# Performance work log

Hardware: AMD Instinct MI355X
Metric: run time of the kernel (lower is better)

## Reference

```python
import jax, jax.numpy as jnp
import numpy as np

EPS = 1e-8  # torch F.cosine_similarity eps
TEMP = 1.0  # temperature k


def setup_inputs() -> dict:
    key = jax.random.key(0)
    k1, k2, k3 = jax.random.split(key, 3)
    B, T, N, D = 16, 4096, 512, 512
    c = jax.random.normal(k1, (B, T, D), dtype=jnp.float32)
    y_t = jax.random.normal(k2, (B, T, D), dtype=jnp.float32)
    y_distraction = jax.random.normal(k3, (B, N, D), dtype=jnp.float32)
    return {"c": c, "y_t": y_t, "y_distraction": y_distraction}


def reference(c, y_t, y_distraction):
    # norms clamped at eps, matching torch F.cosine_similarity
    n_c = jnp.maximum(jnp.linalg.norm(c, axis=-1), EPS)            # [B,T]
    n_t = jnp.maximum(jnp.linalg.norm(y_t, axis=-1), EPS)          # [B,T]
    n_d = jnpp_norm = jnp.maximum(jnp.linalg.norm(y_distraction, axis=-1), EPS)  # [B,N]

    # positive similarity and exp
    q_t = jnp.exp(jnp.sum(y_t * c, axis=-1) / (n_t * n_c) / TEMP)  # [B,T]

    # distractor cosine similarities via einsum (avoids [B,T,N,D] broadcast)
    scores = jnp.einsum('btd,bnd->btn', c, y_distraction)          # [B,T,N]
    scores = scores / (n_c[:, :, None] * n_d[:, None, :])
    q_distraction = jnp.sum(jnp.exp(scores / TEMP), axis=2) + q_t  # [B,T]

    loss = -jnp.sum(jnp.log(q_t / q_distraction))                  # scalar
    return loss
```

## Files before the change

### kernel.cpp

```cpp
#include <hip/hip_runtime.h>
#include <hip/hip_bf16.h>

#define B_   16
#define T_   4096
#define N_   512
#define D_   512
#define EPSF 1e-8f

typedef __attribute__((ext_vector_type(8))) short bf16x8;
typedef __attribute__((ext_vector_type(4))) float f32x4;

__device__ __forceinline__ unsigned int pack2bf(float a, float b) {
  unsigned int ua = __float_as_uint(a);
  ua += 0x7fffu + ((ua >> 16) & 1u);
  unsigned int ub = __float_as_uint(b);
  ub += 0x7fffu + ((ub >> 16) & 1u);
  return (ua >> 16) | (ub & 0xffff0000u);
}

__device__ __forceinline__ void gload_lds16(const void* g, void* l) {
  __builtin_amdgcn_global_load_lds(
      (const __attribute__((address_space(1))) unsigned int*)g,
      (__attribute__((address_space(3))) unsigned int*)l, 16, 0, 0);
}

__global__ void rownorms_d(const float* __restrict__ yd,
                           float* __restrict__ inv_nd,
                           unsigned short* __restrict__ ydbf) {
  const int tid = threadIdx.x;
  const int g   = tid >> 4;
  const int t   = tid & 15;
  const int row = blockIdx.x * 16 + g;
  const float* dr = yd + (size_t)row * D_;
  unsigned short* ob = ydbf + (size_t)row * D_;

  float dd = 0.f;
#pragma unroll
  for (int k = 0; k < 8; ++k) {
    const int col = k * 64 + t * 4;
    float4 a = *(const float4*)(dr + col);
    dd += a.x * a.x + a.y * a.y + a.z * a.z + a.w * a.w;
    uint2 p;
    p.x = pack2bf(a.x, a.y);
    p.y = pack2bf(a.z, a.w);
    *(uint2*)(ob + col) = p;
  }
#pragma unroll
  for (int m = 1; m < 16; m <<= 1) dd += __shfl_xor(dd, m);
  if (t == 0) inv_nd[row] = 1.f / fmaxf(sqrtf(dd), EPSF);
}

__launch_bounds__(512, 2)
__global__ void fused_ct(const float* __restrict__ c,
                         const float* __restrict__ yt,
                         const unsigned short* __restrict__ ydbf,
                         const float* __restrict__ inv_nd,
                         float* __restrict__ rt,
                         float* __restrict__ S) {
  __shared__ __align__(16) unsigned char As[128 * 64 * 2];
  __shared__ __align__(16) unsigned char Bs[512 * 64 * 2];
  __shared__ float s_invc[128];
  __shared__ float s_invd[512];

  const int mt = blockIdx.x;
  const int b  = blockIdx.y;
  const int tid  = threadIdx.x;
  const int lane = tid & 63;
  const int w    = tid >> 6;
  const int wm   = w >> 2, wn = w & 3;

  const float* Ab = c  + ((size_t)b * T_ + (size_t)mt * 128) * D_;
  const float* Tb = yt + ((size_t)b * T_ + (size_t)mt * 128) * D_;
  const unsigned short* Bb = ydbf + (size_t)b * N_ * D_;

#pragma unroll
  for (int j = 0; j < 8; ++j) {
    const int g   = j * 512 + tid;
    const int row = g >> 3;
    const int sch = (g & 7) ^ (row & 7);
    gload_lds16(Bb + (size_t)row * D_ + (sch << 3), Bs + (g << 4));
  }

  s_invd[tid] = inv_nd[b * N_ + tid];

  {
    const int t  = tid & 15;
    const int rg = tid >> 4;
#pragma unroll
    for (int rp = 0; rp < 4; ++rp) {
      const int row = rp * 32 + rg;
      const float* cr = Ab + (size_t)row * D_;
      const float* tr = Tb + (size_t)row * D_;
      float cc = 0.f, tt = 0.f, ct = 0.f;
#pragma unroll
      for (int k = 0; k < 8; ++k) {
        const int col = k * 64 + t * 4;
        float4 a  = *(const float4*)(cr + col);
        float4 bb = *(const float4*)(tr + col);
        cc += a.x * a.x + a.y * a.y + a.z * a.z + a.w * a.w;
        tt += bb.x * bb.x + bb.y * bb.y + bb.z * bb.z + bb.w * bb.w;
        ct += a.x * bb.x + a.y * bb.y + a.z * bb.z + a.w * bb.w;
      }
#pragma unroll
      for (int m = 1; m < 16; m <<= 1) {
        cc += __shfl_xor(cc, m);
        tt += __shfl_xor(tt, m);
        ct += __shfl_xor(ct, m);
      }
      if (t == 0) {
        float nc = fmaxf(sqrtf(cc), EPSF);
        float nt = fmaxf(sqrtf(tt), EPSF);
        s_invc[row] = 1.f / nc;
        rt[b * T_ + mt * 128 + row] = ct / (nt * nc);
      }
    }
  }

  f32x4 acc[4][8] = {};

  for (int k0i = 0; k0i < 8; ++k0i) {
    const int k0 = k0i * 64;
#pragma unroll
    for (int j = 0; j < 4; ++j) {
      const int g   = j * 512 + tid;
      const int row = g >> 4;
      const int c4  = g & 15;
      const float4 va = *(const float4*)(Ab + (size_t)row * D_ + k0 + (c4 << 2));
      const int off = (row << 7) + ((((c4 >> 1) ^ (row & 7))) << 4) + ((c4 & 1) << 3);
      uint2 pa;
      pa.x = pack2bf(va.x, va.y);
      pa.y = pack2bf(va.z, va.w);
      *(uint2*)(As + off) = pa;
    }
    if (k0i > 0) {
#pragma unroll
      for (int j = 0; j < 8; ++j) {
        const int g   = j * 512 + tid;
        const int row = g >> 3;
        const int sch = (g & 7) ^ (row & 7);
        gload_lds16(Bb + (size_t)row * D_ + k0 + (sch << 3), Bs + (g << 4));
      }
    }
    __syncthreads();

#pragma unroll
    for (int ks = 0; ks < 2; ++ks) {
      bf16x8 af[4], bfr[8];
#pragma unroll
      for (int i = 0; i < 4; ++i) {
        const int ar  = wm * 64 + i * 16 + (lane & 15);
        const int ach = (ks * 4 + (lane >> 4)) ^ (ar & 7);
        af[i] = *(const bf16x8*)(As + (ar << 7) + (ach << 4));
      }
#pragma unroll
      for (int n = 0; n < 8; ++n) {
        const int br  = wn * 128 + n * 16 + (lane & 15);
        const int bch = (ks * 4 + (lane >> 4)) ^ (br & 7);
        bfr[n] = *(const bf16x8*)(Bs + (br << 7) + (bch << 4));
      }
#pragma unroll
      for (int mi = 0; mi < 4; ++mi)
#pragma unroll
        for (int ni = 0; ni < 8; ++ni)
          acc[mi][ni] = __builtin_amdgcn_mfma_f32_16x16x32_bf16(
              af[mi], bfr[ni], acc[mi][ni], 0, 0, 0);
    }
    __syncthreads();
  }

  float invd[8];
#pragma unroll
  for (int ni = 0; ni < 8; ++ni)
    invd[ni] = s_invd[wn * 128 + ni * 16 + (lane & 15)];

#pragma unroll
  for (int mi = 0; mi < 4; ++mi) {
    const int t0l = wm * 64 + mi * 16 + ((lane >> 4) << 2);
#pragma unroll
    for (int r = 0; r < 4; ++r) {
      const float invc = s_invc[t0l + r];
      float s = 0.f;
#pragma unroll
      for (int ni = 0; ni < 8; ++ni)
        s += __expf(acc[mi][ni][r] * invc * invd[ni]);
      s += __shfl_xor(s, 1);
      s += __shfl_xor(s, 2);
      s += __shfl_xor(s, 4);
      s += __shfl_xor(s, 8);
      if ((lane & 15) == 0)
        atomicAdd(&S[b * T_ + mt * 128 + t0l + r], s);
    }
  }
}

__global__ void final_loss(const float* __restrict__ S,
                           const float* __restrict__ rt,
                           float* __restrict__ out) {
  const int tid = threadIdx.x;
  float sum = 0.f;
  for (int i = blockIdx.x * blockDim.x + tid; i < B_ * T_;
       i += gridDim.x * blockDim.x) {
    const float r = rt[i];
    sum += logf(S[i] + __expf(r)) - r;
  }
#pragma unroll
  for (int m = 32; m; m >>= 1) sum += __shfl_xor(sum, m);
  __shared__ float ws[4];
  if ((tid & 63) == 0) ws[tid >> 6] = sum;
  __syncthreads();
  if (tid == 0) atomicAdd(out, ws[0] + ws[1] + ws[2] + ws[3]);
}

extern "C" void kernel_launch(void* const* d_in, const int* in_sizes, int n_in,
                              void* d_out, int out_size, void* d_ws, size_t ws_size,
                              hipStream_t stream) {
  (void)in_sizes; (void)n_in; (void)out_size; (void)ws_size;
  const float* c  = (const float*)d_in[0];
  const float* yt = (const float*)d_in[1];
  const float* yd = (const float*)d_in[2];
  float* out = (float*)d_out;

  const size_t ydbf_n = (size_t)B_ * N_ * D_;
  unsigned short* ydbf = (unsigned short*)d_ws;
  float* rt     = (float*)(ydbf + ydbf_n);
  float* inv_nd = rt + B_ * T_;
  float* S      = inv_nd + B_ * N_;

  hipMemsetAsync(S, 0, (size_t)B_ * T_ * sizeof(float), stream);
  hipMemsetAsync(out, 0, sizeof(float), stream);

  rownorms_d<<<B_ * N_ / 16, 256, 0, stream>>>(yd, inv_nd, ydbf);

  dim3 gF(T_ / 128, B_);
  fused_ct<<<gF, 512, 0, stream>>>(c, yt, ydbf, inv_nd, rt, S);

  final_loss<<<64, 256, 0, stream>>>(S, rt, out);
}
```

Before: 111.2 us.

## Double-buffer B tiles, prefetch A/T in registers, fuse row stats into GEMM loop

```diff
diff --git a/kernel.cpp b/kernel.cpp
--- a/kernel.cpp
+++ b/kernel.cpp
@@ -50,6 +50,53 @@
   if (t == 0) inv_nd[row] = 1.f / fmaxf(sqrtf(dd), EPSF);
 }
 
+__device__ __forceinline__ void stage_B(unsigned char* Bsbuf,
+                                        const unsigned short* __restrict__ Bb,
+                                        int k0, int tid) {
+#pragma unroll
+  for (int j = 0; j < 8; ++j) {
+    const int g   = j * 512 + tid;
+    const int row = g >> 3;
+    const int sch = (g & 7) ^ (row & 7);
+    gload_lds16(Bb + (size_t)row * D_ + k0 + (sch << 3), Bsbuf + (g << 4));
+  }
+}
+
+__device__ __forceinline__ void load_AT(const float* __restrict__ Ab,
+                                        const float* __restrict__ Tb,
+                                        int k0, int tid,
+                                        float4* va, float4* vb) {
+#pragma unroll
+  for (int j = 0; j < 4; ++j) {
+    const int g   = j * 512 + tid;
+    const int row = g >> 4;
+    const int c4  = g & 15;
+    const size_t off = (size_t)row * D_ + k0 + (c4 << 2);
+    va[j] = *(const float4*)(Ab + off);
+    vb[j] = *(const float4*)(Tb + off);
+  }
+}
+
+__device__ __forceinline__ void writeA_stats(unsigned char* As,
+                                             const float4* va, const float4* vb,
+                                             int tid,
+                                             float* cc, float* tt, float* ct) {
+#pragma unroll
+  for (int j = 0; j < 4; ++j) {
+    const int g   = j * 512 + tid;
+    const int row = g >> 4;
+    const int c4  = g & 15;
+    const int off = (row << 7) + ((((c4 >> 1) ^ (row & 7))) << 4) + ((c4 & 1) << 3);
+    uint2 pa;
+    pa.x = pack2bf(va[j].x, va[j].y);
+    pa.y = pack2bf(va[j].z, va[j].w);
+    *(uint2*)(As + off) = pa;
+    cc[j] += va[j].x * va[j].x + va[j].y * va[j].y + va[j].z * va[j].z + va[j].w * va[j].w;
+    tt[j] += vb[j].x * vb[j].x + vb[j].y * vb[j].y + vb[j].z * vb[j].z + vb[j].w * vb[j].w;
+    ct[j] += va[j].x * vb[j].x + va[j].y * vb[j].y + va[j].z * vb[j].z + va[j].w * vb[j].w;
+  }
+}
+
 __launch_bounds__(512, 2)
 __global__ void fused_ct(const float* __restrict__ c,
                          const float* __restrict__ yt,
@@ -58,7 +105,7 @@
                          float* __restrict__ rt,
                          float* __restrict__ S) {
   __shared__ __align__(16) unsigned char As[128 * 64 * 2];
-  __shared__ __align__(16) unsigned char Bs[512 * 64 * 2];
+  __shared__ __align__(16) unsigned char Bs[2][512 * 64 * 2];
   __shared__ float s_invc[128];
   __shared__ float s_invd[512];
 
@@ -73,75 +120,26 @@
   const float* Tb = yt + ((size_t)b * T_ + (size_t)mt * 128) * D_;
   const unsigned short* Bb = ydbf + (size_t)b * N_ * D_;
 
-#pragma unroll
-  for (int j = 0; j < 8; ++j) {
-    const int g   = j * 512 + tid;
-    const int row = g >> 3;
-    const int sch = (g & 7) ^ (row & 7);
-    gload_lds16(Bb + (size_t)row * D_ + (sch << 3), Bs + (g << 4));
-  }
-
+  float4 va[4], vb[4];
+  float cc[4] = {0.f, 0.f, 0.f, 0.f};
+  float tt[4] = {0.f, 0.f, 0.f, 0.f};
+  float ct[4] = {0.f, 0.f, 0.f, 0.f};
+
+  stage_B(Bs[0], Bb, 0, tid);
+  load_AT(Ab, Tb, 0, tid, va, vb);
   s_invd[tid] = inv_nd[b * N_ + tid];
-
-  {
-    const int t  = tid & 15;
-    const int rg = tid >> 4;
-#pragma unroll
-    for (int rp = 0; rp < 4; ++rp) {
-      const int row = rp * 32 + rg;
-      const float* cr = Ab + (size_t)row * D_;
-      const float* tr = Tb + (size_t)row * D_;
-      float cc = 0.f, tt = 0.f, ct = 0.f;
-#pragma unroll
-      for (int k = 0; k < 8; ++k) {
-        const int col = k * 64 + t * 4;
-        float4 a  = *(const float4*)(cr + col);
-        float4 bb = *(const float4*)(tr + col);
-        cc += a.x * a.x + a.y * a.y + a.z * a.z + a.w * a.w;
-        tt += bb.x * bb.x + bb.y * bb.y + bb.z * bb.z + bb.w * bb.w;
-        ct += a.x * bb.x + a.y * bb.y + a.z * bb.z + a.w * bb.w;
-      }
-#pragma unroll
-      for (int m = 1; m < 16; m <<= 1) {
-        cc += __shfl_xor(cc, m);
-        tt += __shfl_xor(tt, m);
-        ct += __shfl_xor(ct, m);
-      }
-      if (t == 0) {
-        float nc = fmaxf(sqrtf(cc), EPSF);
-        float nt = fmaxf(sqrtf(tt), EPSF);
-        s_invc[row] = 1.f / nc;
-        rt[b * T_ + mt * 128 + row] = ct / (nt * nc);
-      }
-    }
-  }
+  writeA_stats(As, va, vb, tid, cc, tt, ct);
+  __syncthreads();
 
   f32x4 acc[4][8] = {};
+  int cur = 0;
 
   for (int k0i = 0; k0i < 8; ++k0i) {
-    const int k0 = k0i * 64;
-#pragma unroll
-    for (int j = 0; j < 4; ++j) {
-      const int g   = j * 512 + tid;
-      const int row = g >> 4;
-      const int c4  = g & 15;
-      const float4 va = *(const float4*)(Ab + (size_t)row * D_ + k0 + (c4 << 2));
-      const int off = (row << 7) + ((((c4 >> 1) ^ (row & 7))) << 4) + ((c4 & 1) << 3);
-      uint2 pa;
-      pa.x = pack2bf(va.x, va.y);
-      pa.y = pack2bf(va.z, va.w);
-      *(uint2*)(As + off) = pa;
-    }
-    if (k0i > 0) {
-#pragma unroll
-      for (int j = 0; j < 8; ++j) {
-        const int g   = j * 512 + tid;
-        const int row = g >> 3;
-        const int sch = (g & 7) ^ (row & 7);
-        gload_lds16(Bb + (size_t)row * D_ + k0 + (sch << 3), Bs + (g << 4));
-      }
-    }
-    __syncthreads();
+    const bool more = (k0i < 7);
+    if (more) {
+      load_AT(Ab, Tb, (k0i + 1) * 64, tid, va, vb);
+      stage_B(Bs[cur ^ 1], Bb, (k0i + 1) * 64, tid);
+    }
 
 #pragma unroll
     for (int ks = 0; ks < 2; ++ks) {
@@ -156,7 +154,7 @@
       for (int n = 0; n < 8; ++n) {
         const int br  = wn * 128 + n * 16 + (lane & 15);
         const int bch = (ks * 4 + (lane >> 4)) ^ (br & 7);
-        bfr[n] = *(const bf16x8*)(Bs + (br << 7) + (bch << 4));
+        bfr[n] = *(const bf16x8*)(Bs[cur] + (br << 7) + (bch << 4));
       }
 #pragma unroll
       for (int mi = 0; mi < 4; ++mi)
@@ -165,8 +163,32 @@
           acc[mi][ni] = __builtin_amdgcn_mfma_f32_16x16x32_bf16(
               af[mi], bfr[ni], acc[mi][ni], 0, 0, 0);
     }
+
     __syncthreads();
-  }
+    if (more) {
+      writeA_stats(As, va, vb, tid, cc, tt, ct);
+      __syncthreads();
+    }
+    cur ^= 1;
+  }
+
+#pragma unroll
+  for (int j = 0; j < 4; ++j) {
+#pragma unroll
+    for (int m = 1; m < 16; m <<= 1) {
+      cc[j] += __shfl_xor(cc[j], m);
+      tt[j] += __shfl_xor(tt[j], m);
+      ct[j] += __shfl_xor(ct[j], m);
+    }
+    if ((tid & 15) == 0) {
+      const int row = j * 32 + (tid >> 4);
+      const float nc = fmaxf(sqrtf(cc[j]), EPSF);
+      const float nt = fmaxf(sqrtf(tt[j]), EPSF);
+      s_invc[row] = 1.f / nc;
+      rt[b * T_ + mt * 128 + row] = ct[j] / (nt * nc);
+    }
+  }
+  __syncthreads();
 
   float invd[8];
 #pragma unroll
```

After: 93.04 us. 16.3% less time.

## Double-buffer LDS tiles, fuse norm pass into GEMM loop, fold final loss in

Applied to the files above, without the earlier changes.

```diff
diff --git a/kernel.cpp b/kernel.cpp
--- a/kernel.cpp
+++ b/kernel.cpp
@@ -9,6 +9,8 @@
 
 typedef __attribute__((ext_vector_type(8))) short bf16x8;
 typedef __attribute__((ext_vector_type(4))) float f32x4;
+
+#define SCHED0 __builtin_amdgcn_sched_barrier(0)
 
 __device__ __forceinline__ unsigned int pack2bf(float a, float b) {
   unsigned int ua = __float_as_uint(a);
@@ -50,20 +52,36 @@
   if (t == 0) inv_nd[row] = 1.f / fmaxf(sqrtf(dd), EPSF);
 }
 
+__device__ __forceinline__ void stage_B(unsigned char* buf,
+                                        const unsigned short* __restrict__ Bb,
+                                        int k0, int tid) {
+#pragma unroll
+  for (int j = 0; j < 8; ++j) {
+    const int g   = j * 512 + tid;
+    const int row = g >> 3;
+    const int sch = (g & 7) ^ (row & 7);
+    gload_lds16(Bb + (size_t)row * D_ + k0 + (sch << 3), buf + (g << 4));
+  }
+}
+
 __launch_bounds__(512, 2)
 __global__ void fused_ct(const float* __restrict__ c,
                          const float* __restrict__ yt,
                          const unsigned short* __restrict__ ydbf,
                          const float* __restrict__ inv_nd,
-                         float* __restrict__ rt,
-                         float* __restrict__ S) {
-  __shared__ __align__(16) unsigned char As[128 * 64 * 2];
-  __shared__ __align__(16) unsigned char Bs[512 * 64 * 2];
+                         float* __restrict__ out) {
+  __shared__ __align__(16) unsigned char Bs[2][512 * 64 * 2];
+  __shared__ __align__(16) unsigned char As[2][128 * 32 * 2];
+  __shared__ float s_invd[512];
   __shared__ float s_invc[128];
-  __shared__ float s_invd[512];
-
-  const int mt = blockIdx.x;
-  const int b  = blockIdx.y;
+  __shared__ float s_rt[128];
+  __shared__ float s_S[128];
+
+  const int bid  = blockIdx.x;
+  const int orig = (bid & 7) * 64 + (bid >> 3);
+  const int b    = orig >> 5;
+  const int mt   = orig & 31;
+
   const int tid  = threadIdx.x;
   const int lane = tid & 63;
   const int w    = tid >> 6;
@@ -73,100 +91,145 @@
   const float* Tb = yt + ((size_t)b * T_ + (size_t)mt * 128) * D_;
   const unsigned short* Bb = ydbf + (size_t)b * N_ * D_;
 
-#pragma unroll
-  for (int j = 0; j < 8; ++j) {
-    const int g   = j * 512 + tid;
-    const int row = g >> 3;
-    const int sch = (g & 7) ^ (row & 7);
-    gload_lds16(Bb + (size_t)row * D_ + (sch << 3), Bs + (g << 4));
-  }
-
+  const int arow = tid >> 2;
+  const int q    = tid & 3;
+  const int xr   = (arow & 3) ^ ((arow >> 2) & 1);
+  unsigned char* As0w = As[0] + (arow << 6) + ((q ^ xr) << 4);
+  unsigned char* As1w = As[1] + (arow << 6) + ((q ^ xr) << 4);
+  const size_t aoff = (size_t)arow * D_ + q * 8;
+
+  float4 c0a, c0b, t0a, t0b;
+  float4 c1a, c1b, t1a, t1b;
+  float cc = 0.f, ttv = 0.f, ctv = 0.f;
+
+  stage_B(Bs[0], Bb, 0, tid);
+  { const float* p = Ab + aoff;       c0a = *(const float4*)p; c0b = *(const float4*)(p + 4);
+    const float* y = Tb + aoff;       t0a = *(const float4*)y; t0b = *(const float4*)(y + 4); }
+  { const float* p = Ab + aoff + 32;  c1a = *(const float4*)p; c1b = *(const float4*)(p + 4);
+    const float* y = Tb + aoff + 32;  t1a = *(const float4*)y; t1b = *(const float4*)(y + 4); }
   s_invd[tid] = inv_nd[b * N_ + tid];
-
+  if (tid < 128) s_S[tid] = 0.f;
   {
-    const int t  = tid & 15;
-    const int rg = tid >> 4;
-#pragma unroll
-    for (int rp = 0; rp < 4; ++rp) {
-      const int row = rp * 32 + rg;
-      const float* cr = Ab + (size_t)row * D_;
-      const float* tr = Tb + (size_t)row * D_;
-      float cc = 0.f, tt = 0.f, ct = 0.f;
-#pragma unroll
-      for (int k = 0; k < 8; ++k) {
-        const int col = k * 64 + t * 4;
-        float4 a  = *(const float4*)(cr + col);
-        float4 bb = *(const float4*)(tr + col);
-        cc += a.x * a.x + a.y * a.y + a.z * a.z + a.w * a.w;
-        tt += bb.x * bb.x + bb.y * bb.y + bb.z * bb.z + bb.w * bb.w;
-        ct += a.x * bb.x + a.y * bb.y + a.z * bb.z + a.w * bb.w;
-      }
-#pragma unroll
-      for (int m = 1; m < 16; m <<= 1) {
-        cc += __shfl_xor(cc, m);
-        tt += __shfl_xor(tt, m);
-        ct += __shfl_xor(ct, m);
-      }
-      if (t == 0) {
-        float nc = fmaxf(sqrtf(cc), EPSF);
-        float nt = fmaxf(sqrtf(tt), EPSF);
-        s_invc[row] = 1.f / nc;
-        rt[b * T_ + mt * 128 + row] = ct / (nt * nc);
-      }
-    }
-  }
+    uint4 v;
+    v.x = pack2bf(c0a.x, c0a.y); v.y = pack2bf(c0a.z, c0a.w);
+    v.z = pack2bf(c0b.x, c0b.y); v.w = pack2bf(c0b.z, c0b.w);
+    *(uint4*)As0w = v;
+    cc  += c0a.x*c0a.x + c0a.y*c0a.y + c0a.z*c0a.z + c0a.w*c0a.w
+         + c0b.x*c0b.x + c0b.y*c0b.y + c0b.z*c0b.z + c0b.w*c0b.w;
+    ttv += t0a.x*t0a.x + t0a.y*t0a.y + t0a.z*t0a.z + t0a.w*t0a.w
+         + t0b.x*t0b.x + t0b.y*t0b.y + t0b.z*t0b.z + t0b.w*t0b.w;
+    ctv += c0a.x*t0a.x + c0a.y*t0a.y + c0a.z*t0a.z + c0a.w*t0a.w
+         + c0b.x*t0b.x + c0b.y*t0b.y + c0b.z*t0b.z + c0b.w*t0b.w;
+  }
+  SCHED0; asm volatile("s_waitcnt lgkmcnt(0)" ::: "memory"); SCHED0;
+  __builtin_amdgcn_s_barrier(); SCHED0;
 
   f32x4 acc[4][8] = {};
-
-  for (int k0i = 0; k0i < 8; ++k0i) {
-    const int k0 = k0i * 64;
-#pragma unroll
-    for (int j = 0; j < 4; ++j) {
-      const int g   = j * 512 + tid;
-      const int row = g >> 4;
-      const int c4  = g & 15;
-      const float4 va = *(const float4*)(Ab + (size_t)row * D_ + k0 + (c4 << 2));
-      const int off = (row << 7) + ((((c4 >> 1) ^ (row & 7))) << 4) + ((c4 & 1) << 3);
-      uint2 pa;
-      pa.x = pack2bf(va.x, va.y);
-      pa.y = pack2bf(va.z, va.w);
-      *(uint2*)(As + off) = pa;
-    }
-    if (k0i > 0) {
-#pragma unroll
-      for (int j = 0; j < 8; ++j) {
-        const int g   = j * 512 + tid;
-        const int row = g >> 3;
-        const int sch = (g & 7) ^ (row & 7);
-        gload_lds16(Bb + (size_t)row * D_ + k0 + (sch << 3), Bs + (g << 4));
-      }
-    }
-    __syncthreads();
-
-#pragma unroll
-    for (int ks = 0; ks < 2; ++ks) {
-      bf16x8 af[4], bfr[8];
-#pragma unroll
-      for (int i = 0; i < 4; ++i) {
-        const int ar  = wm * 64 + i * 16 + (lane & 15);
-        const int ach = (ks * 4 + (lane >> 4)) ^ (ar & 7);
-        af[i] = *(const bf16x8*)(As + (ar << 7) + (ach << 4));
-      }
-#pragma unroll
-      for (int n = 0; n < 8; ++n) {
-        const int br  = wn * 128 + n * 16 + (lane & 15);
-        const int bch = (ks * 4 + (lane >> 4)) ^ (br & 7);
-        bfr[n] = *(const bf16x8*)(Bs + (br << 7) + (bch << 4));
-      }
-#pragma unroll
-      for (int mi = 0; mi < 4; ++mi)
-#pragma unroll
-        for (int ni = 0; ni < 8; ++ni)
-          acc[mi][ni] = __builtin_amdgcn_mfma_f32_16x16x32_bf16(
-              af[mi], bfr[ni], acc[mi][ni], 0, 0, 0);
-    }
-    __syncthreads();
-  }
+  const int kc = lane >> 4;
+
+#pragma unroll 1
+  for (int t = 0; t < 8; ++t) {
+    const unsigned char* Bcur = Bs[t & 1];
+    unsigned char* Bnxt = Bs[(t + 1) & 1];
+
+    if (t < 7) {
+      const float* p = Ab + aoff + (t + 1) * 64;
+      const float* y = Tb + aoff + (t + 1) * 64;
+      c0a = *(const float4*)p; c0b = *(const float4*)(p + 4);
+      t0a = *(const float4*)y; t0b = *(const float4*)(y + 4);
+      stage_B(Bnxt, Bb, (t + 1) * 64, tid);
+    }
+    bf16x8 af[4], bfr[8];
+#pragma unroll
+    for (int i = 0; i < 4; ++i) {
+      const int ar = wm * 64 + i * 16 + (lane & 15);
+      const int xa = (ar & 3) ^ ((ar >> 2) & 1);
+      af[i] = *(const bf16x8*)(As[0] + (ar << 6) + ((kc ^ xa) << 4));
+    }
+#pragma unroll
+    for (int n = 0; n < 8; ++n) {
+      const int br = wn * 128 + n * 16 + (lane & 15);
+      bfr[n] = *(const bf16x8*)(Bcur + (br << 7) + ((kc ^ (br & 7)) << 4));
+    }
+    {
+      uint4 v;
+      v.x = pack2bf(c1a.x, c1a.y); v.y = pack2bf(c1a.z, c1a.w);
+      v.z = pack2bf(c1b.x, c1b.y); v.w = pack2bf(c1b.z, c1b.w);
+      *(uint4*)As1w = v;
+      cc  += c1a.x*c1a.x + c1a.y*c1a.y + c1a.z*c1a.z + c1a.w*c1a.w
+           + c1b.x*c1b.x + c1b.y*c1b.y + c1b.z*c1b.z + c1b.w*c1b.w;
+      ttv += t1a.x*t1a.x + t1a.y*t1a.y + t1a.z*t1a.z + t1a.w*t1a.w
+           + t1b.x*t1b.x + t1b.y*t1b.y + t1b.z*t1b.z + t1b.w*t1b.w;
+      ctv += c1a.x*t1a.x + c1a.y*t1a.y + c1a.z*t1a.z + c1a.w*t1a.w
+           + c1b.x*t1b.x + c1b.y*t1b.y + c1b.z*t1b.z + c1b.w*t1b.w;
+    }
+    SCHED0; asm volatile("s_waitcnt lgkmcnt(0)" ::: "memory"); SCHED0;
+    __builtin_amdgcn_s_barrier(); SCHED0;
+    __builtin_amdgcn_s_setprio(1);
+#pragma unroll
+    for (int mi = 0; mi < 4; ++mi)
+#pragma unroll
+      for (int ni = 0; ni < 8; ++ni)
+        acc[mi][ni] = __builtin_amdgcn_mfma_f32_16x16x32_bf16(
+            af[mi], bfr[ni], acc[mi][ni], 0, 0, 0);
+    __builtin_amdgcn_s_setprio(0);
+    SCHED0; __builtin_amdgcn_s_barrier(); SCHED0;
+
+    if (t < 7) {
+      const float* p = Ab + aoff + (t + 1) * 64 + 32;
+      const float* y = Tb + aoff + (t + 1) * 64 + 32;
+      c1a = *(const float4*)p; c1b = *(const float4*)(p + 4);
+      t1a = *(const float4*)y; t1b = *(const float4*)(y + 4);
+    }
+#pragma unroll
+    for (int i = 0; i < 4; ++i) {
+      const int ar = wm * 64 + i * 16 + (lane & 15);
+      const int xa = (ar & 3) ^ ((ar >> 2) & 1);
+      af[i] = *(const bf16x8*)(As[1] + (ar << 6) + ((kc ^ xa) << 4));
+    }
+#pragma unroll
+    for (int n = 0; n < 8; ++n) {
+      const int br = wn * 128 + n * 16 + (lane & 15);
+      bfr[n] = *(const bf16x8*)(Bcur + (br << 7) + (((4 + kc) ^ (br & 7)) << 4));
+    }
+    if (t < 7) {
+      uint4 v;
+      v.x = pack2bf(c0a.x, c0a.y); v.y = pack2bf(c0a.z, c0a.w);
+      v.z = pack2bf(c0b.x, c0b.y); v.w = pack2bf(c0b.z, c0b.w);
+      *(uint4*)As0w = v;
+      cc  += c0a.x*c0a.x + c0a.y*c0a.y + c0a.z*c0a.z + c0a.w*c0a.w
+           + c0b.x*c0b.x + c0b.y*c0b.y + c0b.z*c0b.z + c0b.w*c0b.w;
+      ttv += t0a.x*t0a.x + t0a.y*t0a.y + t0a.z*t0a.z + t0a.w*t0a.w
+           + t0b.x*t0b.x + t0b.y*t0b.y + t0b.z*t0b.z + t0b.w*t0b.w;
+      ctv += c0a.x*t0a.x + c0a.y*t0a.y + c0a.z*t0a.z + c0a.w*t0a.w
+           + c0b.x*t0b.x + c0b.y*t0b.y + c0b.z*t0b.z + c0b.w*t0b.w;
+    }
+    SCHED0;
+    if (t < 7) asm volatile("s_waitcnt vmcnt(4) lgkmcnt(0)" ::: "memory");
+    else       asm volatile("s_waitcnt vmcnt(0) lgkmcnt(0)" ::: "memory");
+    SCHED0;
+    __builtin_amdgcn_s_barrier(); SCHED0;
+    __builtin_amdgcn_s_setprio(1);
+#pragma unroll
+    for (int mi = 0; mi < 4; ++mi)
+#pragma unroll
+      for (int ni = 0; ni < 8; ++ni)
+        acc[mi][ni] = __builtin_amdgcn_mfma_f32_16x16x32_bf16(
+            af[mi], bfr[ni], acc[mi][ni], 0, 0, 0);
+    __builtin_amdgcn_s_setprio(0);
+    SCHED0; __builtin_amdgcn_s_barrier(); SCHED0;
+  }
+
+  cc  += __shfl_xor(cc, 1);  cc  += __shfl_xor(cc, 2);
+  ttv += __shfl_xor(ttv, 1); ttv += __shfl_xor(ttv, 2);
+  ctv += __shfl_xor(ctv, 1); ctv += __shfl_xor(ctv, 2);
+  if (q == 0) {
+    const float nc = fmaxf(sqrtf(cc), EPSF);
+    const float nt = fmaxf(sqrtf(ttv), EPSF);
+    s_invc[arow] = 1.f / nc;
+    s_rt[arow]   = ctv / (nt * nc);
+  }
+  __syncthreads();
 
   float invd[8];
 #pragma unroll
@@ -187,28 +250,18 @@
       s += __shfl_xor(s, 2);
       s += __shfl_xor(s, 4);
       s += __shfl_xor(s, 8);
-      if ((lane & 15) == 0)
-        atomicAdd(&S[b * T_ + mt * 128 + t0l + r], s);
-    }
-  }
-}
-
-__global__ void final_loss(const float* __restrict__ S,
-                           const float* __restrict__ rt,
-                           float* __restrict__ out) {
-  const int tid = threadIdx.x;
-  float sum = 0.f;
-  for (int i = blockIdx.x * blockDim.x + tid; i < B_ * T_;
-       i += gridDim.x * blockDim.x) {
-    const float r = rt[i];
-    sum += logf(S[i] + __expf(r)) - r;
-  }
-#pragma unroll
-  for (int m = 32; m; m >>= 1) sum += __shfl_xor(sum, m);
-  __shared__ float ws[4];
-  if ((tid & 63) == 0) ws[tid >> 6] = sum;
+      if ((lane & 15) == 0) atomicAdd(&s_S[t0l + r], s);
+    }
+  }
   __syncthreads();
-  if (tid == 0) atomicAdd(out, ws[0] + ws[1] + ws[2] + ws[3]);
+
+  if (tid < 128) {
+    const float r = s_rt[tid];
+    float term = logf(s_S[tid] + __expf(r)) - r;
+#pragma unroll
+    for (int m = 1; m < 64; m <<= 1) term += __shfl_xor(term, m);
+    if ((tid & 63) == 0) atomicAdd(out, term);
+  }
 }
 
 extern "C" void kernel_launch(void* const* d_in, const int* in_sizes, int n_in,
@@ -222,17 +275,11 @@
 
   const size_t ydbf_n = (size_t)B_ * N_ * D_;
   unsigned short* ydbf = (unsigned short*)d_ws;
-  float* rt     = (float*)(ydbf + ydbf_n);
-  float* inv_nd = rt + B_ * T_;
-  float* S      = inv_nd + B_ * N_;
-
-  hipMemsetAsync(S, 0, (size_t)B_ * T_ * sizeof(float), stream);
+  float* inv_nd = (float*)(ydbf + ydbf_n);
+
   hipMemsetAsync(out, 0, sizeof(float), stream);
 
   rownorms_d<<<B_ * N_ / 16, 256, 0, stream>>>(yd, inv_nd, ydbf);
 
-  dim3 gF(T_ / 128, B_);
-  fused_ct<<<gF, 512, 0, stream>>>(c, yt, ydbf, inv_nd, rt, S);
-
-  final_loss<<<64, 256, 0, stream>>>(S, rt, out);
-}
+  fused_ct<<<512, 512, 0, stream>>>(c, yt, ydbf, inv_nd, out);
+}
```

Result: slower. 130.5 us (+17.4%).
